# Performance work log

Measured on AMD Instinct MI355X. Metric: run time of the kernel, lower is better.

## Reference

```python
import jax, jax.numpy as jnp
import numpy as np

MAX_PTS_NORM = 10.0


def setup_inputs() -> dict:
    key = jax.random.key(0)
    k1, k2, k3, k4, k5, k6, k7 = jax.random.split(key, 7)
    N, M, C = 200000, 32, 4
    features = jax.random.normal(k1, (N, M, C), dtype=jnp.float32)
    num_points = jax.random.randint(k2, (N,), 0, 33, dtype=jnp.int64)
    coors = jax.random.randint(k3, (N, 4), 0, 400, dtype=jnp.int64)
    # MLP params: Linear(5,16) -> ReLU -> Linear(16,1)
    W1 = jax.random.normal(k4, (5, 16), dtype=jnp.float32) * (1.0 / np.sqrt(5))
    b1 = jax.random.normal(k5, (16,), dtype=jnp.float32) * 0.01
    W2 = jax.random.normal(k6, (16, 1), dtype=jnp.float32) * (1.0 / np.sqrt(16))
    b2 = jax.random.normal(k7, (1,), dtype=jnp.float32) * 0.01
    return {"features": features, "num_points": num_points, "coors": coors,
            "W1": W1, "b1": b1, "W2": W2, "b2": b2}


def reference(features, num_points, coors, W1, b1, W2, b2):
    N, M, C = features.shape
    npf = num_points.astype(jnp.float32)
    p_density = (jnp.clip(npf, None, MAX_PTS_NORM) / MAX_PTS_NORM)[:, None]  # (N,1)
    xyz = features[:, :, :3]  # (N,M,3)
    mask = (jnp.arange(M)[None, :] < num_points[:, None]).astype(jnp.float32)[:, :, None]  # (N,M,1)
    denom = jnp.clip(npf, 1.0, None)[:, None]  # (N,1)
    sum_xyz = jnp.sum(xyz * mask, axis=1)  # (N,3)
    mean_xyz = sum_xyz / denom  # (N,3)
    diff = (xyz - mean_xyz[:, None, :]) * mask  # (N,M,3)
    var_xyz = jnp.sum(diff * diff, axis=1) / denom  # (N,3)
    var_xyz_mean = jnp.mean(var_xyz, axis=1, keepdims=True)  # (N,1)
    p_var = jnp.exp(-0.5 * var_xyz_mean)  # (N,1)
    mlp_input = jnp.concatenate([p_density, p_var, mean_xyz], axis=1)  # (N,5)
    h = jax.nn.relu(mlp_input @ W1 + b1)  # (N,16)
    logits = h @ W2 + b2  # (N,1)
    return jax.nn.sigmoid(logits)
```

## Files before the change

### kernel.cpp

```cpp
#include <hip/hip_runtime.h>
#include <math.h>


#define VOX_PER_BLOCK 8

__global__ __launch_bounds__(256) void vfe_kernel(
    const float4* __restrict__ feats,
    const int*    __restrict__ num_points,
    const float*  __restrict__ W1,
    const float*  __restrict__ b1,
    const float*  __restrict__ W2,
    const float*  __restrict__ b2,
    float*        __restrict__ out,
    int N)
{
    __shared__ float sW1[80];
    __shared__ float sb1[16];
    __shared__ float sW2[16];
    __shared__ float sb2;

    const int t = threadIdx.x;
    if (t < 80) sW1[t] = W1[t];
    if (t < 16) { sb1[t] = b1[t]; sW2[t] = W2[t]; }
    if (t == 0) sb2 = b2[0];
    __syncthreads();

    const int group = t >> 5;
    const int lane  = t & 31;
    const int vox   = blockIdx.x * VOX_PER_BLOCK + group;
    if (vox >= N) return;

    const int   np        = num_points[vox];
    const float npf       = (float)np;
    const float inv_denom = 1.0f / fmaxf(npf, 1.0f);

    const float4 f = feats[(size_t)vox * 32 + lane];
    const float  m = (lane < np) ? 1.0f : 0.0f;

    float sx = f.x * m, sy = f.y * m, sz = f.z * m;
    #pragma unroll
    for (int d = 16; d >= 1; d >>= 1) {
        sx += __shfl_xor(sx, d, 32);
        sy += __shfl_xor(sy, d, 32);
        sz += __shfl_xor(sz, d, 32);
    }
    const float mean_x = sx * inv_denom;
    const float mean_y = sy * inv_denom;
    const float mean_z = sz * inv_denom;

    const float dx = (f.x - mean_x) * m;
    const float dy = (f.y - mean_y) * m;
    const float dz = (f.z - mean_z) * m;
    float q = dx * dx + dy * dy + dz * dz;
    #pragma unroll
    for (int d = 16; d >= 1; d >>= 1) {
        q += __shfl_xor(q, d, 32);
    }
    const float var_mean  = q * inv_denom * (1.0f / 3.0f);
    const float p_var     = expf(-0.5f * var_mean);
    const float p_density = fminf(npf, 10.0f) * 0.1f;

    float c = 0.0f;
    if (lane < 16) {
        float h = sb1[lane]
                + p_density * sW1[lane]
                + p_var     * sW1[16 + lane]
                + mean_x    * sW1[32 + lane]
                + mean_y    * sW1[48 + lane]
                + mean_z    * sW1[64 + lane];
        h = fmaxf(h, 0.0f);
        c = h * sW2[lane];
    }
    #pragma unroll
    for (int d = 8; d >= 1; d >>= 1) {
        c += __shfl_xor(c, d, 32);
    }

    if (lane == 0) {
        const float logit = c + sb2;
        out[vox] = 1.0f / (1.0f + expf(-logit));
    }
}

extern "C" void kernel_launch(void* const* d_in, const int* in_sizes, int n_in,
                              void* d_out, int out_size, void* d_ws, size_t ws_size,
                              hipStream_t stream) {
    const float4* feats      = (const float4*)d_in[0];
    const int*    num_points = (const int*)d_in[1];
    const float*  W1 = (const float*)d_in[3];
    const float*  b1 = (const float*)d_in[4];
    const float*  W2 = (const float*)d_in[5];
    const float*  b2 = (const float*)d_in[6];
    float* out = (float*)d_out;

    const int N = in_sizes[1];
    const int blocks = (N + VOX_PER_BLOCK - 1) / VOX_PER_BLOCK;
    vfe_kernel<<<blocks, 256, 0, stream>>>(feats, num_points, W1, b1, W2, b2, out, N);
}
```

Before: 166.5 us.

## Use 8 lanes per voxel with single-pass mean/variance reduction

```diff
diff --git a/kernel.cpp b/kernel.cpp
--- a/kernel.cpp
+++ b/kernel.cpp
@@ -2,7 +2,8 @@
 #include <math.h>
 
 
-#define VOX_PER_BLOCK 8
+#define LANES_PER_VOX 8
+#define VOX_PER_BLOCK 32
 
 __global__ __launch_bounds__(256) void vfe_kernel(
     const float4* __restrict__ feats,
@@ -25,60 +26,70 @@
     if (t == 0) sb2 = b2[0];
     __syncthreads();
 
-    const int group = t >> 5;
-    const int lane  = t & 31;
-    const int vox   = blockIdx.x * VOX_PER_BLOCK + group;
+    const int j   = t & 7;
+    const int vox = blockIdx.x * VOX_PER_BLOCK + (t >> 3);
     if (vox >= N) return;
 
     const int   np        = num_points[vox];
     const float npf       = (float)np;
     const float inv_denom = 1.0f / fmaxf(npf, 1.0f);
 
-    const float4 f = feats[(size_t)vox * 32 + lane];
-    const float  m = (lane < np) ? 1.0f : 0.0f;
+    const float4* vbase = feats + (size_t)vox * 32;
+    const float4 f0 = vbase[j];
+    const float4 f1 = vbase[j + 8];
+    const float4 f2 = vbase[j + 16];
+    const float4 f3 = vbase[j + 24];
 
-    float sx = f.x * m, sy = f.y * m, sz = f.z * m;
+    const float m0 = (j      < np) ? 1.0f : 0.0f;
+    const float m1 = (j + 8  < np) ? 1.0f : 0.0f;
+    const float m2 = (j + 16 < np) ? 1.0f : 0.0f;
+    const float m3 = (j + 24 < np) ? 1.0f : 0.0f;
+
+    float sx = f0.x * m0 + f1.x * m1 + f2.x * m2 + f3.x * m3;
+    float sy = f0.y * m0 + f1.y * m1 + f2.y * m2 + f3.y * m3;
+    float sz = f0.z * m0 + f1.z * m1 + f2.z * m2 + f3.z * m3;
+    float sq = m0 * (f0.x * f0.x + f0.y * f0.y + f0.z * f0.z)
+             + m1 * (f1.x * f1.x + f1.y * f1.y + f1.z * f1.z)
+             + m2 * (f2.x * f2.x + f2.y * f2.y + f2.z * f2.z)
+             + m3 * (f3.x * f3.x + f3.y * f3.y + f3.z * f3.z);
+
     #pragma unroll
-    for (int d = 16; d >= 1; d >>= 1) {
-        sx += __shfl_xor(sx, d, 32);
-        sy += __shfl_xor(sy, d, 32);
-        sz += __shfl_xor(sz, d, 32);
+    for (int d = 1; d <= 4; d <<= 1) {
+        sx += __shfl_xor(sx, d);
+        sy += __shfl_xor(sy, d);
+        sz += __shfl_xor(sz, d);
+        sq += __shfl_xor(sq, d);
     }
+
     const float mean_x = sx * inv_denom;
     const float mean_y = sy * inv_denom;
     const float mean_z = sz * inv_denom;
 
-    const float dx = (f.x - mean_x) * m;
-    const float dy = (f.y - mean_y) * m;
-    const float dz = (f.z - mean_z) * m;
-    float q = dx * dx + dy * dy + dz * dz;
-    #pragma unroll
-    for (int d = 16; d >= 1; d >>= 1) {
-        q += __shfl_xor(q, d, 32);
-    }
-    const float var_mean  = q * inv_denom * (1.0f / 3.0f);
-    const float p_var     = expf(-0.5f * var_mean);
+    float qtot = sq - (sx * sx + sy * sy + sz * sz) * inv_denom;
+    float var_mean = fmaxf(qtot, 0.0f) * inv_denom * (1.0f / 3.0f);
+
+    const float p_var     = __expf(-0.5f * var_mean);
     const float p_density = fminf(npf, 10.0f) * 0.1f;
 
     float c = 0.0f;
-    if (lane < 16) {
-        float h = sb1[lane]
-                + p_density * sW1[lane]
-                + p_var     * sW1[16 + lane]
-                + mean_x    * sW1[32 + lane]
-                + mean_y    * sW1[48 + lane]
-                + mean_z    * sW1[64 + lane];
-        h = fmaxf(h, 0.0f);
-        c = h * sW2[lane];
+    #pragma unroll
+    for (int u0 = 0; u0 < 16; u0 += 8) {
+        const int u = u0 + j;
+        float h = sb1[u]
+                + p_density * sW1[u]
+                + p_var     * sW1[16 + u]
+                + mean_x    * sW1[32 + u]
+                + mean_y    * sW1[48 + u]
+                + mean_z    * sW1[64 + u];
+        c += fmaxf(h, 0.0f) * sW2[u];
     }
-    #pragma unroll
-    for (int d = 8; d >= 1; d >>= 1) {
-        c += __shfl_xor(c, d, 32);
-    }
+    c += __shfl_xor(c, 1);
+    c += __shfl_xor(c, 2);
+    c += __shfl_xor(c, 4);
 
-    if (lane == 0) {
+    if (j == 0) {
         const float logit = c + sb2;
-        out[vox] = 1.0f / (1.0f + expf(-logit));
+        out[vox] = 1.0f / (1.0f + __expf(-logit));
     }
 }
 
```

Result: faster. 156.0 us (-6.3%).
